# Kernel tuning notes

Measured on AMD Instinct MI355X. Metric: run time of the kernel, lower is better.

The kernel has to match this reference:

```python
import jax, jax.numpy as jnp
import numpy as np

N = 100000
E = 1600000
NODE_DIM = 64
H = 128
NUM_LAYERS = 3
NUM_CLASSES = 6
NUM_GRAPHS = 512
LN_EPS = 1e-5


def setup_inputs() -> dict:
    key = jax.random.key(0)
    ks = jax.random.split(key, 16)
    s = 0.05
    x = jax.random.normal(ks[0], (N, NODE_DIM), jnp.float32)
    edge_index = jax.random.randint(ks[1], (2, E), 0, N, dtype=jnp.int64)
    batch = jnp.sort(jax.random.randint(ks[2], (N,), 0, NUM_GRAPHS, dtype=jnp.int64))
    return {
        "x": x,
        "edge_index": edge_index,
        "batch": batch,
        "proj_w": jax.random.normal(ks[3], (NODE_DIM, H), jnp.float32) * s,
        "proj_b": jnp.zeros((H,), jnp.float32),
        "lin_l_w": jax.random.normal(ks[4], (NUM_LAYERS, H, H), jnp.float32) * s,
        "lin_l_b": jnp.zeros((NUM_LAYERS, H), jnp.float32),
        "lin_r_w": jax.random.normal(ks[5], (NUM_LAYERS, H, H), jnp.float32) * s,
        "ln_g": jnp.ones((NUM_LAYERS, H), jnp.float32),
        "ln_b": jnp.zeros((NUM_LAYERS, H), jnp.float32),
        "gate_w1": jax.random.normal(ks[6], (H, H // 2), jnp.float32) * s,
        "gate_b1": jnp.zeros((H // 2,), jnp.float32),
        "gate_w2": jax.random.normal(ks[7], (H // 2, 1), jnp.float32) * s,
        "gate_b2": jnp.zeros((1,), jnp.float32),
        "cls_w1": jax.random.normal(ks[8], (H, H // 2), jnp.float32) * s,
        "cls_b1": jnp.zeros((H // 2,), jnp.float32),
        "cls_w2": jax.random.normal(ks[9], (H // 2, NUM_CLASSES), jnp.float32) * s,
        "cls_b2": jnp.zeros((NUM_CLASSES,), jnp.float32),
    }


def _layer_norm(x, g, b):
    mu = jnp.mean(x, axis=-1, keepdims=True)
    var = jnp.mean(jnp.square(x - mu), axis=-1, keepdims=True)
    return (x - mu) * jax.lax.rsqrt(var + LN_EPS) * g + b


def _sage_mean_aggr(x, src, dst):
    # mean of source node features grouped by destination node
    summed = jax.ops.segment_sum(x[src], dst, num_segments=N)  # [N,H]
    deg = jax.ops.segment_sum(jnp.ones((E,), x.dtype), dst, num_segments=N)
    return summed / jnp.maximum(deg, 1.0)[:, None]


def reference(x, edge_index, batch, proj_w, proj_b, lin_l_w, lin_l_b, lin_r_w,
              ln_g, ln_b, gate_w1, gate_b1, gate_w2, gate_b2,
              cls_w1, cls_b1, cls_w2, cls_b2):
    src, dst = edge_index[0], edge_index[1]
    h = jax.nn.relu(x @ proj_w + proj_b)  # [N,H]
    for l in range(NUM_LAYERS):
        r = h
        aggr = _sage_mean_aggr(h, src, dst)
        # PyG SAGEConv: lin_l(aggregated) + lin_r(self), bias only in lin_l
        h = aggr @ lin_l_w[l] + lin_l_b[l] + h @ lin_r_w[l]
        h = _layer_norm(h, ln_g[l], ln_b[l])
        h = jax.nn.elu(h)
        h = h + r  # dropout is identity in eval mode
    # GlobalAttention pooling: segment softmax over nodes per graph
    gate = (jax.nn.relu(h @ gate_w1 + gate_b1) @ gate_w2 + gate_b2)[:, 0]  # [N]
    gmax = jax.ops.segment_max(gate, batch, num_segments=NUM_GRAPHS)
    eg = jnp.exp(gate - gmax[batch])
    denom = jax.ops.segment_sum(eg, batch, num_segments=NUM_GRAPHS)
    alpha = eg / denom[batch]  # [N]
    pooled = jax.ops.segment_sum(h * alpha[:, None], batch, num_segments=NUM_GRAPHS)  # [G,H]
    out = jax.nn.relu(pooled @ cls_w1 + cls_b1) @ cls_w2 + cls_b2  # [G,C]
    return out
```

## Files before the change

kernel.cpp:

```cpp
#include <hip/hip_runtime.h>
#include <hip/hip_fp16.h>
#include <math.h>

#define N_NODES   100000
#define N_EDGES   1600000
#define NDIM      64
#define H         128
#define NUM_LAYERS 3
#define NUM_CLASSES 6
#define NUM_GRAPHS 512
#define LN_EPS    1e-5f
#define NBKT      391
#define SCAP      5376
#define BPAD      136
#define NBLK_AGGR 1280

typedef _Float16 f16x8 __attribute__((ext_vector_type(8)));
typedef float    f32x4 __attribute__((ext_vector_type(4)));

__device__ __forceinline__ int idx_at(const int* raw, int is64, int i) {
    return is64 ? raw[2 * (long long)i] : raw[i];
}
__device__ __forceinline__ int lower_bound(const int* a, int n, int v) {
    int lo = 0, hi = n;
    while (lo < hi) { int m = (lo + hi) >> 1; if (a[m] < v) lo = m + 1; else hi = m; }
    return lo;
}

__global__ void k_detect(const int* eraw, const int* braw, int* flags) {
    if (threadIdx.x == 0 && blockIdx.x == 0) {
        int e64 = 1;
        for (int i = 1; i < 128; i += 2) if (eraw[i] != 0) { e64 = 0; break; }
        flags[0] = e64;
        flags[1] = (braw[N_NODES - 1] == 0) ? 1 : 0;
    }
}

__global__ void k_init(int* bcnt, float* gate_z) {
    int i = blockIdx.x * blockDim.x + threadIdx.x;
    if (i < 512) bcnt[i] = 0;
    if (i < 64) gate_z[i] = 0.f;
}

__global__ void k_conv_batch(const int* braw, const int* flags, int* batch32) {
    int i = blockIdx.x * blockDim.x + threadIdx.x;
    if (i < N_NODES) batch32[i] = idx_at(braw, flags[1], i);
}

__global__ __launch_bounds__(256) void k_bhist(const int* eraw, const int* flags, int* bcnt) {
    __shared__ int c[512];
    int tid = threadIdx.x;
    for (int i = tid; i < 512; i += 256) c[i] = 0;
    __syncthreads();
    int f = flags[0];
    int stride = gridDim.x * 256;
    for (int e = blockIdx.x * 256 + tid; e < N_EDGES; e += stride) {
        int d = idx_at(eraw, f, N_EDGES + e);
        atomicAdd(&c[d >> 8], 1);
    }
    __syncthreads();
    for (int i = tid; i < 512; i += 256) if (c[i]) atomicAdd(&bcnt[i], c[i]);
}

__global__ void k_bscan(const int* bcnt, int* boff, int* bcursor) {
    __shared__ int sh[512];
    int tid = threadIdx.x;
    int v = bcnt[tid];
    sh[tid] = v;
    __syncthreads();
    for (int off = 1; off < 512; off <<= 1) {
        int u = (tid >= off) ? sh[tid - off] : 0;
        __syncthreads();
        sh[tid] += u;
        __syncthreads();
    }
    int excl = sh[tid] - v;
    boff[tid] = excl;
    bcursor[tid] = excl;
    if (tid == 511) boff[512] = sh[511];
}

#define EPB 4096
__global__ __launch_bounds__(256) void k_bucket(const int* eraw, const int* flags,
                                                int* bcursor, unsigned int* br) {
    __shared__ int cnt[512];
    __shared__ int lcur[512];
    int tid = threadIdx.x;
    int f = flags[0];
    int base = blockIdx.x * EPB;
    int se[16], de[16];
#pragma unroll
    for (int j = 0; j < 16; ++j) {
        int e = base + j * 256 + tid;
        if (e < N_EDGES) {
            se[j] = idx_at(eraw, f, e);
            de[j] = idx_at(eraw, f, N_EDGES + e);
        } else de[j] = -1;
    }
    for (int i = tid; i < 512; i += 256) cnt[i] = 0;
    __syncthreads();
#pragma unroll
    for (int j = 0; j < 16; ++j)
        if (de[j] >= 0) atomicAdd(&cnt[de[j] >> 8], 1);
    __syncthreads();
    for (int i = tid; i < 512; i += 256)
        lcur[i] = cnt[i] ? atomicAdd(&bcursor[i], cnt[i]) : 0;
    __syncthreads();
#pragma unroll
    for (int j = 0; j < 16; ++j)
        if (de[j] >= 0) {
            int pos = atomicAdd(&lcur[de[j] >> 8], 1);
            br[pos] = ((unsigned int)(de[j] & 255) << 24) | (unsigned int)se[j];
        }
}

__global__ __launch_bounds__(256) void k_csr_tail(const unsigned int* br, const int* boff,
                                                  int* rowptr, int* col) {
    __shared__ int d256[256];
    __shared__ int sc[256];
    __shared__ int cbuf[SCAP];
    int b = blockIdx.x;
    int tid = threadIdx.x;
    int lo = boff[b], hi = boff[b + 1];
    int wsize = hi - lo;
    d256[tid] = 0;
    __syncthreads();
    for (int i = lo + tid; i < hi; i += 256)
        atomicAdd(&d256[br[i] >> 24], 1);
    __syncthreads();
    int v = d256[tid];
    sc[tid] = v;
    __syncthreads();
    for (int off = 1; off < 256; off <<= 1) {
        int u = (tid >= off) ? sc[tid - off] : 0;
        __syncthreads();
        sc[tid] += u;
        __syncthreads();
    }
    int excl = sc[tid] - v;
    int node = (b << 8) + tid;
    if (node < N_NODES) rowptr[node] = lo + excl;
    if (b == NBKT - 1 && tid == 0) rowptr[N_NODES] = N_EDGES;
    __syncthreads();
    d256[tid] = excl;
    __syncthreads();
    if (wsize <= SCAP) {
        for (int i = lo + tid; i < hi; i += 256) {
            unsigned int r = br[i];
            int p = atomicAdd(&d256[r >> 24], 1);
            cbuf[p] = (int)(r & 0xFFFFFF);
        }
        __syncthreads();
        for (int j = tid; j < wsize; j += 256) col[lo + j] = cbuf[j] << 8;
    } else {
        for (int i = lo + tid; i < hi; i += 256) {
            unsigned int r = br[i];
            int p = atomicAdd(&d256[r >> 24], 1);
            col[lo + p] = (int)(r & 0xFFFFFF) << 8;
        }
    }
}

__global__ void k_prepw(const float* __restrict__ lin_l_w, const float* __restrict__ lin_r_w,
                        const float* __restrict__ gate_w1,
                        __half* __restrict__ W16t, __half* __restrict__ W16g) {
    int i = blockIdx.x * 256 + threadIdx.x;
    if (i < NUM_LAYERS * 128 * 256) {
        int l = i >> 15;
        int rem = i & 32767;
        int n = rem >> 8;
        int k = rem & 255;
        float v = (k < 128) ? lin_l_w[(size_t)l * 16384 + k * 128 + n]
                            : lin_r_w[(size_t)l * 16384 + (k - 128) * 128 + n];
        W16t[(size_t)l * 32768 + n * 256 + k] = __float2half(v);
    } else if (i < NUM_LAYERS * 128 * 256 + 64 * 128) {
        int idx = i - NUM_LAYERS * 128 * 256;
        int n = idx >> 7;
        int k = idx & 127;
        W16g[n * 128 + k] = __float2half(gate_w1[k * 64 + n]);
    }
}

__global__ __launch_bounds__(256) void k_gemm_proj(const float* __restrict__ A,
                                                   const float* __restrict__ W,
                                                   const float* __restrict__ bias,
                                                   __half* __restrict__ C16,
                                                   int nrows, int K) {
    __shared__ float As_t[32][68];
    __shared__ float Ws[32 * 128];
    int tid = threadIdx.x;
    int row0 = blockIdx.x * 64;
    int tr = tid >> 4;
    int tc = tid & 15;
    int c0 = tc * 8;
    float acc[4][8];
#pragma unroll
    for (int i = 0; i < 4; ++i)
#pragma unroll
        for (int j = 0; j < 8; ++j) acc[i][j] = 0.f;

    for (int kc = 0; kc < K; kc += 32) {
        __syncthreads();
#pragma unroll
        for (int it = 0; it < 2; ++it) {
            int idx = tid + it * 256;
            int r = idx >> 3, c4 = idx & 7;
            int gr = row0 + r;
            float4 v = make_float4(0.f, 0.f, 0.f, 0.f);
            if (gr < nrows) v = *(const float4*)(A + (size_t)gr * K + kc + c4 * 4);
            As_t[c4 * 4 + 0][r] = v.x;
            As_t[c4 * 4 + 1][r] = v.y;
            As_t[c4 * 4 + 2][r] = v.z;
            As_t[c4 * 4 + 3][r] = v.w;
        }
#pragma unroll
        for (int it = 0; it < 4; ++it) {
            int idx = tid + it * 256;
            int r = idx >> 5, c4 = idx & 31;
            *(float4*)(&Ws[r * 128 + c4 * 4]) = *(const float4*)(W + (size_t)(kc + r) * 128 + c4 * 4);
        }
        __syncthreads();
#pragma unroll
        for (int k = 0; k < 32; ++k) {
            float4 a4 = *(const float4*)(&As_t[k][tr * 4]);
            float a[4] = {a4.x, a4.y, a4.z, a4.w};
            float4 w0 = *(const float4*)(&Ws[k * 128 + c0]);
            float4 w1 = *(const float4*)(&Ws[k * 128 + c0 + 4]);
            float w[8] = {w0.x, w0.y, w0.z, w0.w, w1.x, w1.y, w1.z, w1.w};
#pragma unroll
            for (int i = 0; i < 4; ++i)
#pragma unroll
                for (int j = 0; j < 8; ++j) acc[i][j] += a[i] * w[j];
        }
    }
    float bv[8];
#pragma unroll
    for (int j = 0; j < 8; ++j) bv[j] = bias[c0 + j];
#pragma unroll
    for (int i = 0; i < 4; ++i) {
        int gr = row0 + tr * 4 + i;
        if (gr < nrows) {
            float o[8];
#pragma unroll
            for (int j = 0; j < 8; ++j) o[j] = fmaxf(acc[i][j] + bv[j], 0.f);
            __half2 p[4];
#pragma unroll
            for (int j = 0; j < 8; j += 2) p[j / 2] = __floats2half2_rn(o[j], o[j + 1]);
            *(float4*)(C16 + (size_t)gr * 128 + c0) = *(float4*)p;
        }
    }
}

__global__ __launch_bounds__(256) void k_gate_mfma(const __half* __restrict__ h16,
                                                   const __half* __restrict__ W16g,
                                                   const float* __restrict__ b1,
                                                   const float* __restrict__ w2,
                                                   const float* __restrict__ b2,
                                                   float* __restrict__ gate) {
    __shared__ __half Bs[64 * BPAD];
    int tid = threadIdx.x;
    int wave = tid >> 6, lane = tid & 63;
    int s = lane & 15, quad = lane >> 4;
    int row0 = blockIdx.x * 64 + wave * 16;
    int arow = row0 + s;
    if (arow >= N_NODES) arow = N_NODES - 1;

#pragma unroll
    for (int it = 0; it < 4; ++it) {
        int idx = tid + it * 256;
        int n = idx >> 4, ch = idx & 15;
        *(float4*)(&Bs[n * BPAD + ch * 8]) = *(const float4*)(W16g + (size_t)n * 128 + ch * 8);
    }
    __syncthreads();

    f32x4 acc[4];
#pragma unroll
    for (int c = 0; c < 4; ++c) acc[c] = (f32x4){0.f, 0.f, 0.f, 0.f};

    const __half* aptr = h16 + (size_t)arow * H;
#pragma unroll
    for (int kc = 0; kc < 128; kc += 32) {
        f16x8 afrag = *(const f16x8*)(aptr + kc + quad * 8);
#pragma unroll
        for (int c = 0; c < 4; ++c) {
            f16x8 bfrag = *(const f16x8*)(&Bs[(c * 16 + s) * BPAD + kc + quad * 8]);
            acc[c] = __builtin_amdgcn_mfma_f32_16x16x32_f16(afrag, bfrag, acc[c], 0, 0, 0);
        }
    }
    float part[4] = {0.f, 0.f, 0.f, 0.f};
#pragma unroll
    for (int c = 0; c < 4; ++c) {
        float bv = b1[c * 16 + s];
        float wv = w2[c * 16 + s];
#pragma unroll
        for (int i = 0; i < 4; ++i)
            part[i] += fmaxf(acc[c][i] + bv, 0.f) * wv;
    }
#pragma unroll
    for (int off = 1; off < 16; off <<= 1) {
#pragma unroll
        for (int i = 0; i < 4; ++i) part[i] += __shfl_xor(part[i], off);
    }
    if (s == 0) {
        float b2v = b2[0];
#pragma unroll
        for (int i = 0; i < 4; ++i) {
            int r = row0 + quad * 4 + i;
            if (r < N_NODES) gate[r] = part[i] + b2v;
        }
    }
}

__global__ __launch_bounds__(64) void k_softmax_g(float* __restrict__ gate,
                                                  const int* __restrict__ batch32,
                                                  float* __restrict__ gsum) {
    int g = blockIdx.x;
    int lane = threadIdx.x;
    int n0 = lower_bound(batch32, N_NODES, g);
    int n1 = lower_bound(batch32, N_NODES, g + 1);
    float m = -INFINITY;
    for (int n = n0 + lane; n < n1; n += 64) m = fmaxf(m, gate[n]);
#pragma unroll
    for (int off = 32; off >= 1; off >>= 1) m = fmaxf(m, __shfl_xor(m, off));
    float s = 0.f;
    for (int n = n0 + lane; n < n1; n += 64) {
        float e = expf(gate[n] - m);
        gate[n] = e;
        s += e;
    }
#pragma unroll
    for (int off = 32; off >= 1; off >>= 1) s += __shfl_xor(s, off);
    if (lane == 0) gsum[g] = s;
}

__global__ __launch_bounds__(256) void k_pool_g(const __half* __restrict__ h16,
                                                const float* __restrict__ eg,
                                                const float* __restrict__ gsum,
                                                const int* __restrict__ batch32,
                                                float* __restrict__ pooled) {
    __shared__ float sacc[256];
    int g = blockIdx.x;
    int tid = threadIdx.x;
    int c = tid & 127;
    int p = tid >> 7;
    int n0 = lower_bound(batch32, N_NODES, g);
    int n1 = lower_bound(batch32, N_NODES, g + 1);
    float acc = 0.f;
    for (int n = n0 + p; n < n1; n += 2)
        acc += eg[n] * __half2float(h16[(size_t)n * H + c]);
    sacc[tid] = acc;
    __syncthreads();
    if (tid < 128) {
        float s = gsum[g];
        float v = sacc[tid] + sacc[tid + 128];
        pooled[(size_t)g * H + tid] = (n1 > n0) ? v / s : 0.f;
    }
}

__global__ __launch_bounds__(256) void k_layer_mfma(const __half* __restrict__ t16,
                                                    __half* __restrict__ h16,
                                                    const __half* __restrict__ W16t,
                                                    const float* __restrict__ bl,
                                                    const float* __restrict__ g,
                                                    const float* __restrict__ bb) {
    __shared__ __half Bs[128 * BPAD];
    int tid = threadIdx.x;
    int wave = tid >> 6, lane = tid & 63;
    int s = lane & 15, quad = lane >> 4;
    int row0 = blockIdx.x * 64;
    int wrow0 = row0 + wave * 16;
    int arow = wrow0 + s;
    if (arow >= N_NODES) arow = N_NODES - 1;

    f32x4 acc[8];
#pragma unroll
    for (int c = 0; c < 8; ++c) acc[c] = (f32x4){0.f, 0.f, 0.f, 0.f};

#pragma unroll
    for (int ph = 0; ph < 2; ++ph) {
        __syncthreads();
#pragma unroll
        for (int it = 0; it < 8; ++it) {
            int idx = tid + it * 256;
            int n = idx >> 4, ch = idx & 15;
            *(float4*)(&Bs[n * BPAD + ch * 8]) =
                *(const float4*)(W16t + (size_t)n * 256 + ph * 128 + ch * 8);
        }
        __syncthreads();
        const __half* aptr = (ph ? h16 : t16) + (size_t)arow * H;
#pragma unroll
        for (int kk = 0; kk < 128; kk += 32) {
            f16x8 afrag = *(const f16x8*)(aptr + kk + quad * 8);
#pragma unroll
            for (int c = 0; c < 8; ++c) {
                f16x8 bfrag = *(const f16x8*)(&Bs[(c * 16 + s) * BPAD + kk + quad * 8]);
                acc[c] = __builtin_amdgcn_mfma_f32_16x16x32_f16(afrag, bfrag, acc[c], 0, 0, 0);
            }
        }
    }

    float y[8][4];
    float sm[4] = {0.f, 0.f, 0.f, 0.f}, sq[4] = {0.f, 0.f, 0.f, 0.f};
#pragma unroll
    for (int c = 0; c < 8; ++c) {
        float bv = bl[c * 16 + s];
#pragma unroll
        for (int i = 0; i < 4; ++i) {
            float v = acc[c][i] + bv;
            y[c][i] = v;
            sm[i] += v;
            sq[i] += v * v;
        }
    }
#pragma unroll
    for (int off = 1; off < 16; off <<= 1) {
#pragma unroll
        for (int i = 0; i < 4; ++i) {
            sm[i] += __shfl_xor(sm[i], off);
            sq[i] += __shfl_xor(sq[i], off);
        }
    }
    float mean[4], rstd[4];
#pragma unroll
    for (int i = 0; i < 4; ++i) {
        mean[i] = sm[i] * (1.0f / H);
        float var = sq[i] * (1.0f / H) - mean[i] * mean[i];
        rstd[i] = rsqrtf(var + LN_EPS);
    }
    float gv[8], bbv[8];
#pragma unroll
    for (int c = 0; c < 8; ++c) { gv[c] = g[c * 16 + s]; bbv[c] = bb[c * 16 + s]; }

    __syncthreads();
#pragma unroll
    for (int i = 0; i < 4; ++i) {
        int lr = wave * 16 + quad * 4 + i;
#pragma unroll
        for (int c = 0; c < 8; ++c) {
            float yv = (y[c][i] - mean[i]) * rstd[i] * gv[c] + bbv[c];
            yv = yv > 0.f ? yv : expf(yv) - 1.f;
            Bs[lr * BPAD + c * 16 + s] = __float2half(yv);
        }
    }
    __syncthreads();
#pragma unroll
    for (int it = 0; it < 4; ++it) {
        int idx = tid + it * 256;
        int r = idx >> 4, ch = idx & 15;
        int grow = row0 + r;
        if (grow < N_NODES) {
            float4 sv = *(float4*)(&Bs[r * BPAD + ch * 8]);
            float4 hv = *(const float4*)(h16 + (size_t)grow * H + ch * 8);
            __half2* pa = (__half2*)&sv;
            const __half2* pb = (const __half2*)&hv;
#pragma unroll
            for (int j = 0; j < 4; ++j) {
                float2 fa = __half22float2(pa[j]);
                float2 fb = __half22float2(pb[j]);
                pa[j] = __floats2half2_rn(fa.x + fb.x, fa.y + fb.y);
            }
            *(float4*)(h16 + (size_t)grow * H + ch * 8) = sv;
        }
    }
}

__global__ __launch_bounds__(256, 5) void k_aggr(const __half* __restrict__ h16,
                                                 const int* __restrict__ rowptr,
                                                 const int* __restrict__ col,
                                                 __half* __restrict__ t16,
                                                 int zoff) {
    int lane = threadIdx.x & 63;
    int wid = blockIdx.x * 4 + (threadIdx.x >> 6);
    const int NW = NBLK_AGGR * 4;
    int s = lane & 15;
    int g = lane >> 4;
    const char* hb = (const char*)h16 + s * 16;

    int node = wid;
    if (node >= N_NODES) return;

    int e0 = rowptr[node];
    int deg = rowptr[node + 1] - e0;
    int cv = (lane < deg) ? col[e0 + lane] : zoff;
    int n1 = node + NW;
    int f0 = 0, ndeg = 0;
    if (n1 < N_NODES) { f0 = rowptr[n1]; ndeg = rowptr[n1 + 1] - f0; }

    while (true) {
        int n2 = n1 + NW;
        int p0 = 0, pdeg = 0;
        if (n2 < N_NODES) { p0 = rowptr[n2]; pdeg = rowptr[n2 + 1] - p0; }
        int ncv = zoff;
        if (n1 < N_NODES && lane < ndeg) ncv = col[f0 + lane];

        __half2 z = __floats2half2_rn(0.f, 0.f);
        __half2 ac[4][4];
#pragma unroll
        for (int a = 0; a < 4; ++a)
#pragma unroll
            for (int k = 0; k < 4; ++k) ac[a][k] = z;

        int r64 = deg < 64 ? deg : 64;
        for (int h32 = 0; h32 < r64; h32 += 32) {
            float4 rv[8];
#pragma unroll
            for (int j = 0; j < 8; ++j) {
                int cb = __shfl(cv, h32 + g + 4 * j);
                rv[j] = *(const float4*)(hb + cb);
            }
#pragma unroll
            for (int j = 0; j < 8; ++j) {
                const __half2* hv = (const __half2*)&rv[j];
                int a = j & 3;
                ac[a][0] = __hadd2(ac[a][0], hv[0]);
                ac[a][1] = __hadd2(ac[a][1], hv[1]);
                ac[a][2] = __hadd2(ac[a][2], hv[2]);
                ac[a][3] = __hadd2(ac[a][3], hv[3]);
            }
        }
        for (int base = 64; base < deg; base += 64) {
            int rem = deg - base;
            int cvv = (lane < rem) ? col[e0 + base + lane] : zoff;
            int rr = rem < 64 ? rem : 64;
            for (int h32 = 0; h32 < rr; h32 += 32) {
                float4 rv[8];
#pragma unroll
                for (int j = 0; j < 8; ++j) {
                    int cb = __shfl(cvv, h32 + g + 4 * j);
                    rv[j] = *(const float4*)(hb + cb);
                }
#pragma unroll
                for (int j = 0; j < 8; ++j) {
                    const __half2* hv = (const __half2*)&rv[j];
                    int a = j & 3;
                    ac[a][0] = __hadd2(ac[a][0], hv[0]);
                    ac[a][1] = __hadd2(ac[a][1], hv[1]);
                    ac[a][2] = __hadd2(ac[a][2], hv[2]);
                    ac[a][3] = __hadd2(ac[a][3], hv[3]);
                }
            }
        }

        float f[8];
#pragma unroll
        for (int k = 0; k < 4; ++k) {
            float2 s0 = __half22float2(ac[0][k]);
            float2 s1 = __half22float2(ac[1][k]);
            float2 s2 = __half22float2(ac[2][k]);
            float2 s3 = __half22float2(ac[3][k]);
            f[2 * k]     = (s0.x + s1.x) + (s2.x + s3.x);
            f[2 * k + 1] = (s0.y + s1.y) + (s2.y + s3.y);
        }
#pragma unroll
        for (int off = 16; off <= 32; off <<= 1) {
#pragma unroll
            for (int k = 0; k < 8; ++k) f[k] += __shfl_xor(f[k], off);
        }
        if (g == 0) {
            float inv = 1.0f / (float)(deg > 1 ? deg : 1);
            __half2 o[4];
#pragma unroll
            for (int k = 0; k < 4; ++k)
                o[k] = __floats2half2_rn(f[2 * k] * inv, f[2 * k + 1] * inv);
            *(float4*)(t16 + (size_t)node * H + s * 8) = *(float4*)o;
        }

        if (n1 >= N_NODES) break;
        node = n1; deg = ndeg; cv = ncv; e0 = f0;
        n1 = n2; f0 = p0; ndeg = pdeg;
    }
}

__global__ __launch_bounds__(64) void k_cls(const float* __restrict__ pooled,
                                            const float* __restrict__ w1,
                                            const float* __restrict__ b1,
                                            const float* __restrict__ w2,
                                            const float* __restrict__ b2,
                                            float* __restrict__ out) {
    __shared__ float sp[64];
    int g = blockIdx.x;
    int lane = threadIdx.x;
    float r0 = pooled[(size_t)g * H + lane];
    float r1 = pooled[(size_t)g * H + 64 + lane];
    float acc = b1[lane];
#pragma unroll 16
    for (int k = 0; k < 64; ++k) acc += __shfl(r0, k) * w1[k * 64 + lane];
#pragma unroll 16
    for (int k = 0; k < 64; ++k) acc += __shfl(r1, k) * w1[(64 + k) * 64 + lane];
    sp[lane] = fmaxf(acc, 0.f);
    __syncthreads();
    if (lane < NUM_CLASSES) {
        float o = b2[lane];
        for (int c = 0; c < 64; ++c) o += sp[c] * w2[c * NUM_CLASSES + lane];
        out[g * NUM_CLASSES + lane] = o;
    }
}

extern "C" void kernel_launch(void* const* d_in, const int* in_sizes, int n_in,
                              void* d_out, int out_size, void* d_ws, size_t ws_size,
                              hipStream_t stream) {
    const float* x       = (const float*)d_in[0];
    const int*   eraw    = (const int*)d_in[1];
    const int*   braw    = (const int*)d_in[2];
    const float* proj_w  = (const float*)d_in[3];
    const float* proj_b  = (const float*)d_in[4];
    const float* lin_l_w = (const float*)d_in[5];
    const float* lin_l_b = (const float*)d_in[6];
    const float* lin_r_w = (const float*)d_in[7];
    const float* ln_g    = (const float*)d_in[8];
    const float* ln_b    = (const float*)d_in[9];
    const float* gate_w1 = (const float*)d_in[10];
    const float* gate_b1 = (const float*)d_in[11];
    const float* gate_w2 = (const float*)d_in[12];
    const float* gate_b2 = (const float*)d_in[13];
    const float* cls_w1  = (const float*)d_in[14];
    const float* cls_b1  = (const float*)d_in[15];
    const float* cls_w2  = (const float*)d_in[16];
    const float* cls_b2  = (const float*)d_in[17];
    float* out = (float*)d_out;

    __half* h16    = (__half*)d_ws;
    __half* t16    = h16 + (size_t)N_NODES * H;
    float*  gate   = (float*)(t16 + (size_t)N_NODES * H);
    float*  gsum   = gate + N_NODES;
    float*  pooled = gsum + NUM_GRAPHS;
    __half* W16t   = (__half*)(pooled + NUM_GRAPHS * H);
    __half* W16g   = W16t + (size_t)NUM_LAYERS * 32768;
    int* flags     = (int*)(W16g + 64 * 128);
    int* col       = flags + 4;
    int* batch32   = col + N_EDGES;
    int* rowptr    = batch32 + N_NODES;
    int* bcnt      = rowptr + N_NODES + 1;
    int* boff      = bcnt + 512;
    int* bcursor   = boff + 513;
    unsigned int* br = (unsigned int*)(bcursor + 512);

    const int zoff = (int)((const char*)gate - (const char*)h16);

    const int nbN = (N_NODES + 255) / 256;
    const int nbE4 = (N_EDGES + EPB - 1) / EPB;
    const int nbG = (N_NODES + 63) / 64;
    const int nbP = (NUM_LAYERS * 128 * 256 + 64 * 128 + 255) / 256;

    k_detect<<<1, 1, 0, stream>>>(eraw, braw, flags);
    k_init<<<2, 256, 0, stream>>>(bcnt, gate);
    k_conv_batch<<<nbN, 256, 0, stream>>>(braw, flags, batch32);
    k_bhist<<<512, 256, 0, stream>>>(eraw, flags, bcnt);
    k_bscan<<<1, 512, 0, stream>>>(bcnt, boff, bcursor);
    k_bucket<<<nbE4, 256, 0, stream>>>(eraw, flags, bcursor, br);
    k_csr_tail<<<NBKT, 256, 0, stream>>>(br, boff, rowptr, col);
    k_prepw<<<nbP, 256, 0, stream>>>(lin_l_w, lin_r_w, gate_w1, W16t, W16g);

    k_gemm_proj<<<nbG, 256, 0, stream>>>(x, proj_w, proj_b, h16, N_NODES, NDIM);

    for (int l = 0; l < NUM_LAYERS; ++l) {
        const float* bl  = lin_l_b + (size_t)l * H;
        const float* gl  = ln_g + (size_t)l * H;
        const float* blb = ln_b + (size_t)l * H;
        k_aggr<<<NBLK_AGGR, 256, 0, stream>>>(h16, rowptr, col, t16, zoff);
        k_layer_mfma<<<nbG, 256, 0, stream>>>(t16, h16, W16t + (size_t)l * 32768, bl, gl, blb);
    }

    k_gate_mfma<<<nbG, 256, 0, stream>>>(h16, W16g, gate_b1, gate_w2, gate_b2, gate);
    k_softmax_g<<<NUM_GRAPHS, 64, 0, stream>>>(gate, batch32, gsum);
    k_pool_g<<<NUM_GRAPHS, 256, 0, stream>>>(h16, gate, gsum, batch32, pooled);
    k_cls<<<NUM_GRAPHS, 64, 0, stream>>>(pooled, cls_w1, cls_b1, cls_w2, cls_b2, out);
}
```

Measured before the change: 501.8 us.

## Launch one wave per node in SAGE aggregation with inline-asm gathers

```diff
diff --git a/kernel.cpp b/kernel.cpp
--- a/kernel.cpp
+++ b/kernel.cpp
@@ -13,7 +13,6 @@
 #define NBKT      391
 #define SCAP      5376
 #define BPAD      136
-#define NBLK_AGGR 1280
 
 typedef _Float16 f16x8 __attribute__((ext_vector_type(8)));
 typedef float    f32x4 __attribute__((ext_vector_type(4)));
@@ -25,6 +24,13 @@
     int lo = 0, hi = n;
     while (lo < hi) { int m = (lo + hi) >> 1; if (a[m] < v) lo = m + 1; else hi = m; }
     return lo;
+}
+
+__device__ __forceinline__ f32x4 gload16(const __half* __restrict__ base, int voff) {
+    f32x4 r;
+    asm volatile("global_load_dwordx4 %0, %1, %2"
+                 : "=v"(r) : "v"(voff), "s"(base));
+    return r;
 }
 
 __global__ void k_detect(const int* eraw, const int* braw, int* flags) {
@@ -464,50 +470,81 @@
     }
 }
 
-__global__ __launch_bounds__(256, 5) void k_aggr(const __half* __restrict__ h16,
-                                                 const int* __restrict__ rowptr,
-                                                 const int* __restrict__ col,
-                                                 __half* __restrict__ t16,
-                                                 int zoff) {
+__global__ __launch_bounds__(256) void k_aggr(const __half* __restrict__ h16,
+                                              const int* __restrict__ rowptr,
+                                              const int* __restrict__ col,
+                                              __half* __restrict__ t16,
+                                              int zoff) {
     int lane = threadIdx.x & 63;
-    int wid = blockIdx.x * 4 + (threadIdx.x >> 6);
-    const int NW = NBLK_AGGR * 4;
+    int node = blockIdx.x * 4 + (threadIdx.x >> 6);
+    if (node >= N_NODES) return;
     int s = lane & 15;
     int g = lane >> 4;
-    const char* hb = (const char*)h16 + s * 16;
-
-    int node = wid;
-    if (node >= N_NODES) return;
-
+    int soff = s * 16;
     int e0 = rowptr[node];
     int deg = rowptr[node + 1] - e0;
-    int cv = (lane < deg) ? col[e0 + lane] : zoff;
-    int n1 = node + NW;
-    int f0 = 0, ndeg = 0;
-    if (n1 < N_NODES) { f0 = rowptr[n1]; ndeg = rowptr[n1 + 1] - f0; }
-
-    while (true) {
-        int n2 = n1 + NW;
-        int p0 = 0, pdeg = 0;
-        if (n2 < N_NODES) { p0 = rowptr[n2]; pdeg = rowptr[n2 + 1] - p0; }
-        int ncv = zoff;
-        if (n1 < N_NODES && lane < ndeg) ncv = col[f0 + lane];
-
-        __half2 z = __floats2half2_rn(0.f, 0.f);
-        __half2 ac[4][4];
-#pragma unroll
-        for (int a = 0; a < 4; ++a)
-#pragma unroll
-            for (int k = 0; k < 4; ++k) ac[a][k] = z;
-
-        int r64 = deg < 64 ? deg : 64;
-        for (int h32 = 0; h32 < r64; h32 += 32) {
-            float4 rv[8];
+
+    if (deg == 0) {
+        if (g == 0) {
+            float4 zz = make_float4(0.f, 0.f, 0.f, 0.f);
+            *(float4*)(t16 + (size_t)node * H + s * 8) = zz;
+        }
+        return;
+    }
+
+    __half2 z = __floats2half2_rn(0.f, 0.f);
+    __half2 ac[4][4];
+#pragma unroll
+    for (int a = 0; a < 4; ++a)
+#pragma unroll
+        for (int k = 0; k < 4; ++k) ac[a][k] = z;
+
+    {
+        int cb[8];
+#pragma unroll
+        for (int j = 0; j < 8; ++j) {
+            int ei = g + 4 * j;
+            cb[j] = col[e0 + (ei < deg ? ei : 0)];
+        }
+#pragma unroll
+        for (int j = 0; j < 8; ++j) {
+            int ei = g + 4 * j;
+            cb[j] = (ei < deg) ? cb[j] : zoff;
+        }
+        f32x4 rv[8];
+#pragma unroll
+        for (int j = 0; j < 8; ++j) rv[j] = gload16(h16, cb[j] + soff);
+        asm volatile("s_waitcnt vmcnt(0)" ::: "memory");
+        __builtin_amdgcn_sched_barrier(0);
+#pragma unroll
+        for (int j = 0; j < 8; ++j) {
+            const __half2* hv = (const __half2*)&rv[j];
+            int a = j & 3;
+            ac[a][0] = __hadd2(ac[a][0], hv[0]);
+            ac[a][1] = __hadd2(ac[a][1], hv[1]);
+            ac[a][2] = __hadd2(ac[a][2], hv[2]);
+            ac[a][3] = __hadd2(ac[a][3], hv[3]);
+        }
+    }
+
+    if (deg > 32) {
+        for (int base = 32; base < deg; base += 32) {
+            int cb[8];
 #pragma unroll
             for (int j = 0; j < 8; ++j) {
-                int cb = __shfl(cv, h32 + g + 4 * j);
-                rv[j] = *(const float4*)(hb + cb);
+                int ei = base + g + 4 * j;
+                cb[j] = col[e0 + (ei < deg ? ei : base)];
             }
+#pragma unroll
+            for (int j = 0; j < 8; ++j) {
+                int ei = base + g + 4 * j;
+                cb[j] = (ei < deg) ? cb[j] : zoff;
+            }
+            f32x4 rv[8];
+#pragma unroll
+            for (int j = 0; j < 8; ++j) rv[j] = gload16(h16, cb[j] + soff);
+            asm volatile("s_waitcnt vmcnt(0)" ::: "memory");
+            __builtin_amdgcn_sched_barrier(0);
 #pragma unroll
             for (int j = 0; j < 8; ++j) {
                 const __half2* hv = (const __half2*)&rv[j];
@@ -518,56 +555,30 @@
                 ac[a][3] = __hadd2(ac[a][3], hv[3]);
             }
         }
-        for (int base = 64; base < deg; base += 64) {
-            int rem = deg - base;
-            int cvv = (lane < rem) ? col[e0 + base + lane] : zoff;
-            int rr = rem < 64 ? rem : 64;
-            for (int h32 = 0; h32 < rr; h32 += 32) {
-                float4 rv[8];
-#pragma unroll
-                for (int j = 0; j < 8; ++j) {
-                    int cb = __shfl(cvv, h32 + g + 4 * j);
-                    rv[j] = *(const float4*)(hb + cb);
-                }
-#pragma unroll
-                for (int j = 0; j < 8; ++j) {
-                    const __half2* hv = (const __half2*)&rv[j];
-                    int a = j & 3;
-                    ac[a][0] = __hadd2(ac[a][0], hv[0]);
-                    ac[a][1] = __hadd2(ac[a][1], hv[1]);
-                    ac[a][2] = __hadd2(ac[a][2], hv[2]);
-                    ac[a][3] = __hadd2(ac[a][3], hv[3]);
-                }
-            }
-        }
-
-        float f[8];
-#pragma unroll
-        for (int k = 0; k < 4; ++k) {
-            float2 s0 = __half22float2(ac[0][k]);
-            float2 s1 = __half22float2(ac[1][k]);
-            float2 s2 = __half22float2(ac[2][k]);
-            float2 s3 = __half22float2(ac[3][k]);
-            f[2 * k]     = (s0.x + s1.x) + (s2.x + s3.x);
-            f[2 * k + 1] = (s0.y + s1.y) + (s2.y + s3.y);
-        }
-#pragma unroll
-        for (int off = 16; off <= 32; off <<= 1) {
-#pragma unroll
-            for (int k = 0; k < 8; ++k) f[k] += __shfl_xor(f[k], off);
-        }
-        if (g == 0) {
-            float inv = 1.0f / (float)(deg > 1 ? deg : 1);
-            __half2 o[4];
-#pragma unroll
-            for (int k = 0; k < 4; ++k)
-                o[k] = __floats2half2_rn(f[2 * k] * inv, f[2 * k + 1] * inv);
-            *(float4*)(t16 + (size_t)node * H + s * 8) = *(float4*)o;
-        }
-
-        if (n1 >= N_NODES) break;
-        node = n1; deg = ndeg; cv = ncv; e0 = f0;
-        n1 = n2; f0 = p0; ndeg = pdeg;
+    }
+
+    float f[8];
+#pragma unroll
+    for (int k = 0; k < 4; ++k) {
+        float2 s0 = __half22float2(ac[0][k]);
+        float2 s1 = __half22float2(ac[1][k]);
+        float2 s2 = __half22float2(ac[2][k]);
+        float2 s3 = __half22float2(ac[3][k]);
+        f[2 * k]     = (s0.x + s1.x) + (s2.x + s3.x);
+        f[2 * k + 1] = (s0.y + s1.y) + (s2.y + s3.y);
+    }
+#pragma unroll
+    for (int off = 16; off <= 32; off <<= 1) {
+#pragma unroll
+        for (int k = 0; k < 8; ++k) f[k] += __shfl_xor(f[k], off);
+    }
+    if (g == 0) {
+        float inv = 1.0f / (float)(deg > 1 ? deg : 1);
+        __half2 o[4];
+#pragma unroll
+        for (int k = 0; k < 4; ++k)
+            o[k] = __floats2half2_rn(f[2 * k] * inv, f[2 * k + 1] * inv);
+        *(float4*)(t16 + (size_t)node * H + s * 8) = *(float4*)o;
     }
 }
 
@@ -639,6 +650,7 @@
 
     const int nbN = (N_NODES + 255) / 256;
     const int nbE4 = (N_EDGES + EPB - 1) / EPB;
+    const int nbW = (N_NODES + 3) / 4;
     const int nbG = (N_NODES + 63) / 64;
     const int nbP = (NUM_LAYERS * 128 * 256 + 64 * 128 + 255) / 256;
 
@@ -657,7 +669,7 @@
         const float* bl  = lin_l_b + (size_t)l * H;
         const float* gl  = ln_g + (size_t)l * H;
         const float* blb = ln_b + (size_t)l * H;
-        k_aggr<<<NBLK_AGGR, 256, 0, stream>>>(h16, rowptr, col, t16, zoff);
+        k_aggr<<<nbW, 256, 0, stream>>>(h16, rowptr, col, t16, zoff);
         k_layer_mfma<<<nbG, 256, 0, stream>>>(t16, h16, W16t + (size_t)l * 32768, bl, gl, blb);
     }
 
```

Measured after the change: 480.4 us. -4.3%, faster.
